# Kernel tuning notes

Hardware: AMD Instinct MI355X
Metric: run time of the kernel (lower is better)

## Reference

```python
import jax, jax.numpy as jnp
import numpy as np

BOUNDS = [0.01, 1.0, 100.0]
STEPS = [128, 128]
ALPHA_C = 0.01          # cfg.renderer.alpha
N_IMPORTANCE = 128      # cfg.renderer.importance_steps
N_RAYS = 65536


def _zvals_log_coarse():
    # matches torch.linspace(log10(b[i]), log10(b[i+1]) - seg/steps[i], steps[i]) per segment
    segs = []
    for i, s in enumerate(STEPS):
        lo = np.log10(BOUNDS[i]); hi = np.log10(BOUNDS[i + 1])
        segs.append(np.linspace(lo, hi - (hi - lo) / s, s, dtype=np.float32))
    return np.concatenate(segs)


def _seg_scale():
    tot = float(sum(STEPS))
    return np.concatenate([np.full(s, s / tot, dtype=np.float32) for s in STEPS])


def setup_inputs() -> dict:
    key = jax.random.key(0)
    k1, k2, k3, k4 = jax.random.split(key, 4)
    sigmas_coarse = jax.random.uniform(k1, (N_RAYS, sum(STEPS)), dtype=jnp.float32) * 5.0
    sigmas_fine = jax.random.uniform(k2, (N_RAYS, N_IMPORTANCE), dtype=jnp.float32) * 5.0
    rgbs_fine = jax.random.uniform(k3, (N_RAYS, N_IMPORTANCE, 3), dtype=jnp.float32)
    bg_color = jax.random.uniform(k4, (3,), dtype=jnp.float32)
    return {"sigmas_coarse": sigmas_coarse, "sigmas_fine": sigmas_fine,
            "rgbs_fine": rgbs_fine, "bg_color": bg_color}


def _weights_from_sigmas(sigmas, z_log):
    # delta[:, :-1] = diff(z_log), last delta = 0 (as in efficient_sampling)
    delta = jnp.concatenate([z_log[:, 1:] - z_log[:, :-1], jnp.zeros_like(z_log[:, :1])], -1)
    alpha = 1.0 - jnp.exp(-sigmas * delta)
    alpha_shift = jnp.concatenate([jnp.zeros_like(alpha[:, :1]), alpha[:, :-1]], -1)
    trans = jnp.cumprod(1.0 - alpha_shift, axis=-1)   # transmittance
    return alpha * trans


def _reweight(weights):
    # pad with zeros, 3-tap max blur, floor by alpha/S, per-segment rescale, normalize
    wpad = jnp.pad(weights, ((0, 0), (1, 1)))
    w = 0.5 * (jnp.maximum(wpad[:, :-2], wpad[:, 1:-1]) + jnp.maximum(wpad[:, 1:-1], wpad[:, 2:]))
    w = w + ALPHA_C / w.shape[-1]
    w = w * jnp.asarray(_seg_scale())
    return w / jnp.sum(w, axis=-1, keepdims=True)


def _sample_pdf(bins, weights, n_samples):
    # weights already normalized -> pdf; deterministic stratified u for reproducibility
    cdf = jnp.cumsum(weights, axis=-1)                     # [N, S]
    u = (jnp.arange(n_samples, dtype=bins.dtype) + 0.5) / n_samples
    u = jnp.broadcast_to(u, (bins.shape[0], n_samples))    # [N, n]
    inds = jax.vmap(lambda c, uu: jnp.searchsorted(c, uu, side='right'))(cdf, u)
    S = bins.shape[-1]
    below = jnp.clip(inds - 1, 0, S - 1)
    above = jnp.clip(inds, 0, S - 1)
    cdf_b = jnp.take_along_axis(cdf, below, -1)
    cdf_a = jnp.take_along_axis(cdf, above, -1)
    bin_b = jnp.take_along_axis(bins, below, -1)
    bin_a = jnp.take_along_axis(bins, above, -1)
    denom = jnp.where(cdf_a - cdf_b < 1e-5, 1.0, cdf_a - cdf_b)
    t = (u - cdf_b) / denom
    return bin_b + t * (bin_a - bin_b)


def reference(sigmas_coarse, sigmas_fine, rgbs_fine, bg_color):
    # --- efficient_sampling (no_grad path) ---
    z_log = jnp.broadcast_to(jnp.asarray(_zvals_log_coarse()), sigmas_coarse.shape)
    w_coarse = _weights_from_sigmas(sigmas_coarse, z_log)
    w_re = _reweight(w_coarse)
    z_log_fine = _sample_pdf(z_log, w_re, N_IMPORTANCE)     # [N, n_imp], sorted
    z_fine = jnp.power(10.0, z_log_fine)
    # --- render_rays_log-style compositing on fine samples ---
    w_fine = _weights_from_sigmas(sigmas_fine, z_log_fine)
    image = jnp.einsum('ns,nsc->nc', w_fine, rgbs_fine)
    image = image + (1.0 - jnp.sum(w_fine, -1)[..., None]) * bg_color
    invdepth = jnp.sum(w_fine / z_fine, axis=-1)
    lo = np.float32(np.log10(BOUNDS[0])); hi = np.float32(np.log10(BOUNDS[-1]))
    z_log_s = (z_log_fine - lo) / (hi - lo)
    return image, invdepth, w_fine, z_log_s
```

## Files before the change

kernel.cpp:

```cpp
#include <hip/hip_runtime.h>

#define SC 256
#define NF 128

template<int CTRL, int RM, int BM>
__device__ __forceinline__ float dpp_add(float x) {
    int s = __builtin_amdgcn_update_dpp(0, __float_as_int(x), CTRL, RM, BM, true);
    return x + __int_as_float(s);
}
template<int CTRL>
__device__ __forceinline__ float dpp_mov0(float x) {
    return __int_as_float(__builtin_amdgcn_update_dpp(0, __float_as_int(x), CTRL, 0xF, 0xF, true));
}
__device__ __forceinline__ float lane_f(float x, int l) {
    return __int_as_float(__builtin_amdgcn_readlane(__float_as_int(x), l));
}

__device__ __forceinline__ float wave_incl_scan(float x) {
    x = dpp_add<0x111, 0xF, 0xF>(x);
    x = dpp_add<0x112, 0xF, 0xF>(x);
    x = dpp_add<0x114, 0xF, 0xF>(x);
    x = dpp_add<0x118, 0xF, 0xF>(x);
    x = dpp_add<0x142, 0xA, 0xF>(x);
    x = dpp_add<0x143, 0xC, 0xF>(x);
    return x;
}

__device__ __forceinline__ float wave_sum_lane0(float x) {
    x = dpp_add<0xB1, 0xF, 0xF>(x);
    x = dpp_add<0x4E, 0xF, 0xF>(x);
    x = dpp_add<0x124, 0xF, 0xF>(x);
    x = dpp_add<0x128, 0xF, 0xF>(x);
    return x + lane_f(x, 16) + lane_f(x, 32) + lane_f(x, 48);
}

__global__ __launch_bounds__(256) void nerf_render_kernel(
    const float* __restrict__ sig_c,
    const float* __restrict__ sig_f,
    const float* __restrict__ rgb_f,
    const float* __restrict__ bg,
    float* __restrict__ out,
    int n_rays)
{
    const int lane = threadIdx.x & 63;
    const int wid  = threadIdx.x >> 6;
    const int ray  = (blockIdx.x << 2) + wid;
    if (ray >= n_rays) return;

    __shared__ float s_cdf[4][SC];

    const float4 sc4 = *reinterpret_cast<const float4*>(sig_c + (size_t)ray * SC + 4 * lane);
    const float DLT = 0.015625f;
    float x0 = sc4.x * DLT;
    float x1 = sc4.y * DLT;
    float x2 = sc4.z * DLT;
    float x3 = (lane == 63) ? 0.0f : sc4.w * DLT;

    float p0 = x0, p1 = p0 + x1, p2 = p1 + x2, p3 = p2 + x3;
    float incl = wave_incl_scan(p3);
    float excl = incl - p3;

    float T0 = __expf(-excl);
    float T1 = __expf(-(excl + p0));
    float T2 = __expf(-(excl + p1));
    float T3 = __expf(-(excl + p2));
    float T4 = __expf(-(excl + p3));
    float w0 = T0 - T1, w1 = T1 - T2, w2 = T2 - T3, w3 = T3 - T4;

    float wl = dpp_mov0<0x138>(w3);
    float wr = dpp_mov0<0x130>(w0);

    const float FLOOR = 0.01f / 256.0f;
    float m01 = fmaxf(w0, w1), m12 = fmaxf(w1, w2), m23 = fmaxf(w2, w3);
    float r0 = 0.5f * (fmaxf(wl, w0) + m01) + FLOOR;
    float r1 = 0.5f * (m01 + m12) + FLOOR;
    float r2 = 0.5f * (m12 + m23) + FLOOR;
    float r3 = 0.5f * (m23 + fmaxf(w3, wr)) + FLOOR;

    float q0 = r0, q1 = q0 + r1, q2 = q1 + r2, q3 = q2 + r3;
    float incl2 = wave_incl_scan(q3);
    float excl2 = incl2 - q3;
    float total = lane_f(incl2, 63);
    float inv_total = __builtin_amdgcn_rcpf(total);

    *reinterpret_cast<float4*>(&s_cdf[wid][4 * lane]) = make_float4(
        (excl2 + q0) * inv_total, (excl2 + q1) * inv_total,
        (excl2 + q2) * inv_total, (excl2 + q3) * inv_total);

    __syncthreads();

    const float* cdf = s_cdf[wid];
    float zl[2];
    #pragma unroll
    for (int s = 0; s < 2; ++s) {
        const int k = 2 * lane + s;
        const float u = ((float)k + 0.5f) * (1.0f / 128.0f);
        int pos = 0;
        #pragma unroll
        for (int step = 128; step >= 1; step >>= 1) {
            if (cdf[pos + step - 1] <= u) pos += step;
        }
        int below = pos - 1; if (below < 0) below = 0;
        int above = pos;     if (above > SC - 1) above = SC - 1;
        float cdf_b = cdf[below];
        float cdf_a = cdf[above];
        float bin_b = -2.0f + (float)below * 0.015625f;
        float bin_a = -2.0f + (float)above * 0.015625f;
        float dn = cdf_a - cdf_b;
        dn = (dn < 1e-5f) ? 1.0f : dn;
        float t = (u - cdf_b) / dn;
        zl[s] = bin_b + t * (bin_a - bin_b);
    }
    float zl0 = zl[0], zl1 = zl[1];

    float znext = dpp_mov0<0x130>(zl0);
    float d0 = zl1 - zl0;
    float d1 = (lane == 63) ? 0.0f : (znext - zl1);

    const float2 sf = *reinterpret_cast<const float2*>(sig_f + (size_t)ray * NF + 2 * lane);
    float y0 = sf.x * d0;
    float y1 = sf.y * d1;
    float ps = y0 + y1;
    float fincl = wave_incl_scan(ps);
    float fexcl = fincl - ps;

    float U0 = __expf(-fexcl);
    float U1 = __expf(-(fexcl + y0));
    float U2 = __expf(-(fexcl + ps));
    float wf0 = U0 - U1, wf1 = U1 - U2;

    const float2* rp = reinterpret_cast<const float2*>(rgb_f + (size_t)ray * (NF * 3) + 6 * lane);
    float2 ra = rp[0], rb = rp[1], rc = rp[2];
    float img_r = wf0 * ra.x + wf1 * rb.y;
    float img_g = wf0 * ra.y + wf1 * rc.x;
    float img_b = wf0 * rb.x + wf1 * rc.y;
    float wsum  = wf0 + wf1;
    float invd = wf0 * __exp10f(-zl0) + wf1 * __exp10f(-zl1);

    img_r = wave_sum_lane0(img_r);
    img_g = wave_sum_lane0(img_g);
    img_b = wave_sum_lane0(img_b);
    wsum  = wave_sum_lane0(wsum);
    invd  = wave_sum_lane0(invd);

    float* out_img  = out;
    float* out_invd = out + (size_t)n_rays * 3;
    float* out_wf   = out + (size_t)n_rays * 4;
    float* out_zs   = out + (size_t)n_rays * 4 + (size_t)n_rays * NF;

    if (lane == 0) {
        float one_m = 1.0f - wsum;
        out_img[(size_t)ray * 3 + 0] = img_r + one_m * bg[0];
        out_img[(size_t)ray * 3 + 1] = img_g + one_m * bg[1];
        out_img[(size_t)ray * 3 + 2] = img_b + one_m * bg[2];
        out_invd[ray] = invd;
    }
    *reinterpret_cast<float2*>(out_wf + (size_t)ray * NF + 2 * lane) =
        make_float2(wf0, wf1);
    *reinterpret_cast<float2*>(out_zs + (size_t)ray * NF + 2 * lane) =
        make_float2((zl0 + 2.0f) * 0.25f, (zl1 + 2.0f) * 0.25f);
}

extern "C" void kernel_launch(void* const* d_in, const int* in_sizes, int n_in,
                              void* d_out, int out_size, void* d_ws, size_t ws_size,
                              hipStream_t stream) {
    const float* sig_c = (const float*)d_in[0];
    const float* sig_f = (const float*)d_in[1];
    const float* rgb_f = (const float*)d_in[2];
    const float* bg    = (const float*)d_in[3];
    float* out = (float*)d_out;

    const int n_rays = in_sizes[1] / NF;
    dim3 grid((n_rays + 3) / 4), block(256);
    hipLaunchKernelGGL(nerf_render_kernel, grid, block, 0, stream,
                       sig_c, sig_f, rgb_f, bg, out, n_rays);
}
```

Before: 233.1 us.

## Replace per-sample CDF binary search with per-bin scatter of fine samples

Instead of each lane binary-searching the shared CDF for its two samples, each lane now walks its four CDF bins and writes the fine sample positions that fall inside each bin into a per-wave shared buffer. The fine sigma, rgb and background loads are also hoisted to the top of the kernel so they overlap with the coarse computation, and the block-wide __syncthreads is dropped in favour of a compiler memory barrier, relying on each wave reading only its own buffer. This removes eight dependent LDS reads per sample but introduces a data-dependent loop with lane divergence. Its behaviour at edge bins (j==0, zero-width bins) may differ slightly from the reference.

```diff
diff --git a/kernel.cpp b/kernel.cpp
--- a/kernel.cpp
+++ b/kernel.cpp
@@ -34,6 +34,23 @@
     return x + lane_f(x, 16) + lane_f(x, 32) + lane_f(x, 48);
 }
 
+__device__ __forceinline__ void scatter_bin(float* __restrict__ zbuf,
+                                            int j, float cl, float cr) {
+    int klo = (int)ceilf(fmaf(128.0f, cl, -0.5f));
+    int khi = (int)ceilf(fmaf(128.0f, cr, -0.5f));
+    if (klo < 0)  klo = 0;
+    if (khi > NF) khi = NF;
+    if (klo >= khi) return;
+    float dn   = cr - cl;
+    float invd = (dn < 1e-5f) ? 1.0f : __builtin_amdgcn_rcpf(dn);
+    float scale = (j == 0) ? 0.0f : 0.015625f;
+    float zL    = (j == 0) ? -2.0f : fmaf((float)(j - 1), 0.015625f, -2.0f);
+    for (int k = klo; k < khi; ++k) {
+        float u = ((float)k + 0.5f) * 0.0078125f;
+        zbuf[k] = fmaf((u - cl) * invd, scale, zL);
+    }
+}
+
 __global__ __launch_bounds__(256) void nerf_render_kernel(
     const float* __restrict__ sig_c,
     const float* __restrict__ sig_f,
@@ -47,9 +64,14 @@
     const int ray  = (blockIdx.x << 2) + wid;
     if (ray >= n_rays) return;
 
-    __shared__ float s_cdf[4][SC];
+    __shared__ float s_z[4][NF];
 
     const float4 sc4 = *reinterpret_cast<const float4*>(sig_c + (size_t)ray * SC + 4 * lane);
+    const float2 sf  = *reinterpret_cast<const float2*>(sig_f + (size_t)ray * NF + 2 * lane);
+    const float2* rp = reinterpret_cast<const float2*>(rgb_f + (size_t)ray * (NF * 3) + 6 * lane);
+    const float2 ra = rp[0], rb = rp[1], rc = rp[2];
+    const float bg0 = bg[0], bg1 = bg[1], bg2 = bg[2];
+
     const float DLT = 0.015625f;
     float x0 = sc4.x * DLT;
     float x1 = sc4.y * DLT;
@@ -83,41 +105,28 @@
     float total = lane_f(incl2, 63);
     float inv_total = __builtin_amdgcn_rcpf(total);
 
-    *reinterpret_cast<float4*>(&s_cdf[wid][4 * lane]) = make_float4(
-        (excl2 + q0) * inv_total, (excl2 + q1) * inv_total,
-        (excl2 + q2) * inv_total, (excl2 + q3) * inv_total);
+    float c0 = (excl2 + q0) * inv_total;
+    float c1 = (excl2 + q1) * inv_total;
+    float c2 = (excl2 + q2) * inv_total;
+    float c3 = (excl2 + q3) * inv_total;
+    float cprev = dpp_mov0<0x138>(c3);
 
-    __syncthreads();
+    float* zbuf = s_z[wid];
+    const int jb = 4 * lane;
+    scatter_bin(zbuf, jb + 0, cprev, c0);
+    scatter_bin(zbuf, jb + 1, c0,    c1);
+    scatter_bin(zbuf, jb + 2, c1,    c2);
+    scatter_bin(zbuf, jb + 3, c2,    c3);
 
-    const float* cdf = s_cdf[wid];
-    float zl[2];
-    #pragma unroll
-    for (int s = 0; s < 2; ++s) {
-        const int k = 2 * lane + s;
-        const float u = ((float)k + 0.5f) * (1.0f / 128.0f);
-        int pos = 0;
-        #pragma unroll
-        for (int step = 128; step >= 1; step >>= 1) {
-            if (cdf[pos + step - 1] <= u) pos += step;
-        }
-        int below = pos - 1; if (below < 0) below = 0;
-        int above = pos;     if (above > SC - 1) above = SC - 1;
-        float cdf_b = cdf[below];
-        float cdf_a = cdf[above];
-        float bin_b = -2.0f + (float)below * 0.015625f;
-        float bin_a = -2.0f + (float)above * 0.015625f;
-        float dn = cdf_a - cdf_b;
-        dn = (dn < 1e-5f) ? 1.0f : dn;
-        float t = (u - cdf_b) / dn;
-        zl[s] = bin_b + t * (bin_a - bin_b);
-    }
-    float zl0 = zl[0], zl1 = zl[1];
+    __asm__ __volatile__("" ::: "memory");
+
+    const float2 zl2 = *reinterpret_cast<const float2*>(&zbuf[2 * lane]);
+    float zl0 = zl2.x, zl1 = zl2.y;
 
     float znext = dpp_mov0<0x130>(zl0);
     float d0 = zl1 - zl0;
     float d1 = (lane == 63) ? 0.0f : (znext - zl1);
 
-    const float2 sf = *reinterpret_cast<const float2*>(sig_f + (size_t)ray * NF + 2 * lane);
     float y0 = sf.x * d0;
     float y1 = sf.y * d1;
     float ps = y0 + y1;
@@ -129,8 +138,6 @@
     float U2 = __expf(-(fexcl + ps));
     float wf0 = U0 - U1, wf1 = U1 - U2;
 
-    const float2* rp = reinterpret_cast<const float2*>(rgb_f + (size_t)ray * (NF * 3) + 6 * lane);
-    float2 ra = rp[0], rb = rp[1], rc = rp[2];
     float img_r = wf0 * ra.x + wf1 * rb.y;
     float img_g = wf0 * ra.y + wf1 * rc.x;
     float img_b = wf0 * rb.x + wf1 * rc.y;
@@ -150,9 +157,9 @@
 
     if (lane == 0) {
         float one_m = 1.0f - wsum;
-        out_img[(size_t)ray * 3 + 0] = img_r + one_m * bg[0];
-        out_img[(size_t)ray * 3 + 1] = img_g + one_m * bg[1];
-        out_img[(size_t)ray * 3 + 2] = img_b + one_m * bg[2];
+        out_img[(size_t)ray * 3 + 0] = img_r + one_m * bg0;
+        out_img[(size_t)ray * 3 + 1] = img_g + one_m * bg1;
+        out_img[(size_t)ray * 3 + 2] = img_b + one_m * bg2;
         out_invd[ray] = invd;
     }
     *reinterpret_cast<float2*>(out_wf + (size_t)ray * NF + 2 * lane) =
```

After: 237.8 us. 1.02x slower.
